# Kernel tuning notes

Hardware: AMD Instinct MI355X
Metric: run time of the kernel (lower is better)

## Reference

```python
import jax, jax.numpy as jnp
import numpy as np

B, C, S, Q = 4, 3, 5, 5
E = 90 * 768          # encoding_size for encoding_method != 1
N1 = B * C * S        # 60 support rows
N2 = B * C * Q        # 60 query rows
H = 32                # width of every Dense layer


def setup_inputs() -> dict:
    key = jax.random.key(0)
    ks = jax.random.split(key, 20)
    p = lambda k, shape: jax.random.normal(k, shape, jnp.float32) * 0.1
    return {
        "support_distance": jax.random.normal(ks[0], (N1, E), jnp.float32),
        "support_label": jax.random.randint(ks[1], (B, 15), 0, C, jnp.int32),
        "query_distance": jax.random.normal(ks[2], (N2, E), jnp.float32),
        # fvc_bar / gvc_bar (shared between distance and label paths)
        "W_fvc_bar": p(ks[3], (1, H)),  "b_fvc_bar": p(ks[4], (H,)),
        "W_gvc_bar": p(ks[5], (H, H)), "b_gvc_bar": p(ks[6], (H,)),
        # fu / gu (input to fu is concat([repeat(32-dim), 1-dim]) -> 33)
        "W_fu": p(ks[7], (H + 1, H)),  "b_fu": p(ks[8], (H,)),
        "W_gu": p(ks[9], (H, H)),      "b_gu": p(ks[10], (H,)),
        # fvc / gvc
        "W_fvc": p(ks[11], (H + 1, H)), "b_fvc": p(ks[12], (H,)),
        "W_gvc": p(ks[13], (H, H)),     "b_gvc": p(ks[14], (H,)),
        # fz / gz
        "W_fz": p(ks[15], (H + 1, H)),  "b_fz": p(ks[16], (H,)),
        "W_gz": p(ks[17], (H, H)),      "b_gz": p(ks[18], (H,)),
    }


def reference(support_distance, support_label, query_distance,
              W_fvc_bar, b_fvc_bar, W_gvc_bar, b_gvc_bar,
              W_fu, b_fu, W_gu, b_gu,
              W_fvc, b_fvc, W_gvc, b_gvc,
              W_fz, b_fz, W_gz, b_gz):
    relu = jax.nn.relu
    d1 = support_distance[..., None]                                   # [N1,E,1]
    # v_bar: fvc_bar over each scalar of the distance, mean over rows, then gvc_bar
    v_bar = relu(jnp.mean(relu(d1 @ W_fvc_bar + b_fvc_bar), axis=0)
                 @ W_gvc_bar + b_gvc_bar)                               # [E,32]
    # c_bar: same stack applied to one-hot labels
    lab = jax.nn.one_hot(support_label.reshape(N1).astype(jnp.int32), C)[..., None]  # [N1,C,1]
    c_bar = relu(jnp.mean(relu(lab @ W_fvc_bar + b_fvc_bar), axis=0)
                 @ W_gvc_bar + b_gvc_bar)                               # [C,32]
    # fu on concat([repeat(v_bar), d1]): split the 33-row weight to avoid concat
    Wu_v, wu_d = W_fu[:H], W_fu[H:]                                     # [32,32],[1,32]
    alpha = jnp.mean(relu((v_bar @ Wu_v)[None] + d1 * wu_d[0] + b_fu), axis=1)  # [N1,32]
    beta = jnp.mean(relu((c_bar @ Wu_v)[None] + lab * wu_d[0] + b_fu), axis=1)  # [N1,32]
    u_n = relu((alpha + beta) @ W_gu + b_gu)                            # [N1,32]
    # fvc on concat([repeat(u_n over E), d1]), mean over rows, gvc
    Wv_u, wv_d = W_fvc[:H], W_fvc[H:]
    v = relu(jnp.mean(relu((u_n @ Wv_u)[:, None, :] + d1 * wv_d[0] + b_fvc),
                      axis=0) @ W_gvc + b_gvc)                          # [E,32]
    # query branch: fz on concat([repeat(v), d2]), mean over E, gz
    d2 = query_distance[..., None]                                      # [N2,E,1]
    Wz_v, wz_d = W_fz[:H], W_fz[H:]
    z = jnp.mean(relu((v @ Wz_v)[None] + d2 * wz_d[0] + b_fz), axis=1)  # [N2,32]
    new_distance = relu(z @ W_gz + b_gz)                                # [N2,32]
    return new_distance.reshape(B, C, Q, H)
```

## Files before the change

### kernel.cpp

```cpp
#include <hip/hip_runtime.h>

#define E_DIM 69120
#define N1 60
#define H 32
#define CC 3
#define TEB 64
#define NB2 (E_DIM / TEB)
#define SDS 65
#define SBT 66
#define PSZ (N1 * H)

#define OFF_R2 (N1 * SDS * 4)
#define OFF_R3 (OFF_R2 + 64 * 33 * 4)
#define SMEM_SZ (OFF_R3 + 64 * 33 * 4)

template<bool ATOMIC>
__global__ __launch_bounds__(256, 4) void kA3(
    const float* __restrict__ d,
    const float* __restrict__ Wfvb, const float* __restrict__ bfvb,
    const float* __restrict__ Wgvb, const float* __restrict__ bgvb,
    const float* __restrict__ Wfu,  const float* __restrict__ bfu,
    float* __restrict__ outp)
{
    __shared__ __align__(16) char smem[SMEM_SZ];
    float* dsf        = (float*)smem;
    float (*bufA)[33] = (float(*)[33])(smem + OFF_R2);
    float (*bufB)[33] = (float(*)[33])(smem + OFF_R3);
    float* bufT       = (float*)(smem + OFF_R2);
    const int tid = threadIdx.x;
    const long sE = (long)blockIdx.x * TEB;

    for (int i = tid; i < N1 * (TEB / 4); i += 256) {
        const int n = i >> 4, c = (i & 15) * 4;
        const float4 v = *(const float4*)(d + (long)n * E_DIM + sE + c);
        float* w = dsf + n * SDS + c;
        w[0] = v.x; w[1] = v.y; w[2] = v.z; w[3] = v.w;
    }
    __syncthreads();

    const int eLoc = tid & 63, h0 = (tid >> 6) * 8;

    {
        float wf[8], bf[8], t1[8];
        #pragma unroll
        for (int j = 0; j < 8; ++j) { wf[j] = Wfvb[h0+j]; bf[j] = bfvb[h0+j]; t1[j] = 0.f; }
        const float* dp = dsf + eLoc;
        #pragma unroll 4
        for (int n = 0; n < N1; ++n) {
            const float dv = dp[n * SDS];
            #pragma unroll
            for (int j = 0; j < 8; ++j) t1[j] += fmaxf(fmaf(dv, wf[j], bf[j]), 0.f);
        }
        #pragma unroll
        for (int j = 0; j < 8; ++j) bufA[eLoc][h0+j] = t1[j] * (1.f / N1);
    }
    __syncthreads();

    {
        float acc[8];
        #pragma unroll
        for (int j = 0; j < 8; ++j) acc[j] = bgvb[h0+j];
        #pragma unroll
        for (int k = 0; k < H; ++k) {
            const float t = bufA[eLoc][k];
            #pragma unroll
            for (int j = 0; j < 8; ++j) acc[j] = fmaf(t, Wgvb[k*H + h0+j], acc[j]);
        }
        #pragma unroll
        for (int j = 0; j < 8; ++j) bufB[eLoc][h0+j] = fmaxf(acc[j], 0.f);
    }
    __syncthreads();

    {
        float acc[8];
        #pragma unroll
        for (int j = 0; j < 8; ++j) acc[j] = bfu[h0+j];
        #pragma unroll
        for (int k = 0; k < H; ++k) {
            const float t = bufB[eLoc][k];
            #pragma unroll
            for (int j = 0; j < 8; ++j) acc[j] = fmaf(t, Wfu[k*H + h0+j], acc[j]);
        }
        #pragma unroll
        for (int j = 0; j < 8; ++j) bufT[(h0+j)*SBT + eLoc] = acc[j];
    }
    __syncthreads();

    if (tid < N1 * 4) {
        const int n = tid >> 2, hb = (tid & 3) * 8;
        float wud[8], acc[8];
        #pragma unroll
        for (int j = 0; j < 8; ++j) { wud[j] = Wfu[H*H + hb + j]; acc[j] = 0.f; }
        const float* drow = d + (long)n * E_DIM + sE;
        for (int e4 = 0; e4 < TEB; e4 += 4) {
            const float4 d4 = *(const float4*)(drow + e4);
            #pragma unroll
            for (int j = 0; j < 8; ++j) {
                const float* wr = bufT + (hb + j) * SBT + e4;
                const float2 wa = *(const float2*)(wr);
                const float2 wb = *(const float2*)(wr + 2);
                acc[j] += fmaxf(fmaf(d4.x, wud[j], wa.x), 0.f)
                        + fmaxf(fmaf(d4.y, wud[j], wa.y), 0.f)
                        + fmaxf(fmaf(d4.z, wud[j], wb.x), 0.f)
                        + fmaxf(fmaf(d4.w, wud[j], wb.y), 0.f);
            }
        }
        if (ATOMIC) {
            float* p = outp + tid * 8;
            #pragma unroll
            for (int j = 0; j < 8; ++j) atomicAdd(&p[j], acc[j]);
        } else {
            float4* p = (float4*)(outp + (long)blockIdx.x * PSZ + tid * 8);
            p[0] = make_float4(acc[0], acc[1], acc[2], acc[3]);
            p[1] = make_float4(acc[4], acc[5], acc[6], acc[7]);
        }
    }
}

template<bool ATOMIC>
__global__ __launch_bounds__(256, 4) void kCf(
    const float* __restrict__ d, const float* __restrict__ d2,
    const float* __restrict__ uwb,
    const float* __restrict__ Wfvc,
    const float* __restrict__ Wgvc, const float* __restrict__ bgvc,
    const float* __restrict__ Wfz,  const float* __restrict__ bfz,
    float* __restrict__ outp)
{
    __shared__ __align__(16) char smem[SMEM_SZ];
    float* dsf        = (float*)smem;
    float (*bufA)[33] = (float(*)[33])(smem + OFF_R2);
    float (*bufB)[33] = (float(*)[33])(smem + OFF_R3);
    float* u_l        = (float*)(smem + OFF_R3);
    float* bufT       = (float*)(smem + OFF_R2);
    const int tid = threadIdx.x;
    const long sE = (long)blockIdx.x * TEB;

    for (int i = tid; i < N1 * (TEB / 4); i += 256) {
        const int n = i >> 4, c = (i & 15) * 4;
        const float4 v = *(const float4*)(d + (long)n * E_DIM + sE + c);
        float* w = dsf + n * SDS + c;
        w[0] = v.x; w[1] = v.y; w[2] = v.z; w[3] = v.w;
    }
    for (int i = tid; i < PSZ / 4; i += 256)
        ((float4*)u_l)[i] = ((const float4*)uwb)[i];
    __syncthreads();

    const int eLoc = tid & 63, h0 = (tid >> 6) * 8;

    {
        float wvd[8], m[8];
        #pragma unroll
        for (int j = 0; j < 8; ++j) { wvd[j] = Wfvc[H*H + h0+j]; m[j] = 0.f; }
        const float* dp = dsf + eLoc;
        #pragma unroll 4
        for (int n = 0; n < N1; ++n) {
            const float dv = dp[n * SDS];
            const float4 u0 = *(const float4*)(u_l + n * H + h0);
            const float4 u1 = *(const float4*)(u_l + n * H + h0 + 4);
            const float ub[8] = {u0.x, u0.y, u0.z, u0.w, u1.x, u1.y, u1.z, u1.w};
            #pragma unroll
            for (int j = 0; j < 8; ++j) m[j] += fmaxf(fmaf(dv, wvd[j], ub[j]), 0.f);
        }
        #pragma unroll
        for (int j = 0; j < 8; ++j) bufA[eLoc][h0+j] = m[j] * (1.f / N1);
    }
    __syncthreads();

    {
        float acc[8];
        #pragma unroll
        for (int j = 0; j < 8; ++j) acc[j] = bgvc[h0+j];
        #pragma unroll
        for (int k = 0; k < H; ++k) {
            const float t = bufA[eLoc][k];
            #pragma unroll
            for (int j = 0; j < 8; ++j) acc[j] = fmaf(t, Wgvc[k*H + h0+j], acc[j]);
        }
        #pragma unroll
        for (int j = 0; j < 8; ++j) bufB[eLoc][h0+j] = fmaxf(acc[j], 0.f);
    }
    __syncthreads();

    {
        float acc[8];
        #pragma unroll
        for (int j = 0; j < 8; ++j) acc[j] = bfz[h0+j];
        #pragma unroll
        for (int k = 0; k < H; ++k) {
            const float t = bufB[eLoc][k];
            #pragma unroll
            for (int j = 0; j < 8; ++j) acc[j] = fmaf(t, Wfz[k*H + h0+j], acc[j]);
        }
        #pragma unroll
        for (int j = 0; j < 8; ++j) bufT[(h0+j)*SBT + eLoc] = acc[j];
    }
    __syncthreads();

    if (tid < N1 * 4) {
        const int n = tid >> 2, hb = (tid & 3) * 8;
        float wzd[8], acc[8];
        #pragma unroll
        for (int j = 0; j < 8; ++j) { wzd[j] = Wfz[H*H + hb + j]; acc[j] = 0.f; }
        const float* drow = d2 + (long)n * E_DIM + sE;
        for (int e4 = 0; e4 < TEB; e4 += 4) {
            const float4 d4 = *(const float4*)(drow + e4);
            #pragma unroll
            for (int j = 0; j < 8; ++j) {
                const float* wr = bufT + (hb + j) * SBT + e4;
                const float2 wa = *(const float2*)(wr);
                const float2 wb = *(const float2*)(wr + 2);
                acc[j] += fmaxf(fmaf(d4.x, wzd[j], wa.x), 0.f)
                        + fmaxf(fmaf(d4.y, wzd[j], wa.y), 0.f)
                        + fmaxf(fmaf(d4.z, wzd[j], wb.x), 0.f)
                        + fmaxf(fmaf(d4.w, wzd[j], wb.y), 0.f);
            }
        }
        if (ATOMIC) {
            float* p = outp + tid * 8;
            #pragma unroll
            for (int j = 0; j < 8; ++j) atomicAdd(&p[j], acc[j]);
        } else {
            float4* p = (float4*)(outp + (long)blockIdx.x * PSZ + tid * 8);
            p[0] = make_float4(acc[0], acc[1], acc[2], acc[3]);
            p[1] = make_float4(acc[4], acc[5], acc[6], acc[7]);
        }
    }
}

__global__ __launch_bounds__(256) void kR(
    const float* __restrict__ part, float* __restrict__ out)
{
    __shared__ float red[16][17];
    const int tid = threadIdx.x;
    const int oLoc = tid & 15, c = tid >> 4;
    const int o = blockIdx.x * 16 + oLoc;
    const int b0 = c * 68;
    const int bN = (NB2 - b0 < 68) ? (NB2 - b0) : 68;
    const float* p = part + (long)b0 * PSZ + o;
    float s = 0.f;
    #pragma unroll 4
    for (int b = 0; b < bN; ++b) s += p[(long)b * PSZ];
    red[c][oLoc] = s;
    __syncthreads();
    if (tid < 16) {
        float t = 0.f;
        #pragma unroll
        for (int ci = 0; ci < 16; ++ci) t += red[ci][tid];
        out[blockIdx.x * 16 + tid] = t;
    }
}

__global__ __launch_bounds__(1024) void kB(
    const float* __restrict__ alphaAcc, const int* __restrict__ label,
    const float* __restrict__ Wfvb, const float* __restrict__ bfvb,
    const float* __restrict__ Wgvb, const float* __restrict__ bgvb,
    const float* __restrict__ Wfu,  const float* __restrict__ bfu,
    const float* __restrict__ Wgu,  const float* __restrict__ bgu,
    const float* __restrict__ Wfvc, const float* __restrict__ bfvc,
    float* __restrict__ uwb)
{
    __shared__ float up_l[N1 * H];
    __shared__ float un_l[N1 * H];
    __shared__ float cb_l[CC * H];
    __shared__ float cw_l[CC * H];
    __shared__ int   cnt[CC];
    const int tid = threadIdx.x;

    if (tid < CC) cnt[tid] = 0;
    __syncthreads();
    if (tid < N1) atomicAdd(&cnt[label[tid]], 1);
    __syncthreads();

    if (tid < CC * H) {
        const int c = tid / H, h = tid % H;
        const float nc = (float)cnt[c];
        float s = bgvb[h];
        #pragma unroll
        for (int k = 0; k < H; ++k) {
            const float t1c = (nc * fmaxf(Wfvb[k] + bfvb[k], 0.f) +
                               ((float)N1 - nc) * fmaxf(bfvb[k], 0.f)) * (1.f / N1);
            s = fmaf(t1c, Wgvb[k * H + h], s);
        }
        cb_l[tid] = fmaxf(s, 0.f);
    }
    __syncthreads();
    if (tid < CC * H) {
        const int c = tid / H, h = tid % H;
        float s = bfu[h];
        #pragma unroll
        for (int k = 0; k < H; ++k) s = fmaf(cb_l[c * H + k], Wfu[k * H + h], s);
        cw_l[tid] = s;
    }
    __syncthreads();
    for (int t = tid; t < N1 * H; t += 1024) {
        const int n = t >> 5, h = t & 31;
        const int ln = label[n];
        const float wud = Wfu[H * H + h];
        float s = 0.f;
        #pragma unroll
        for (int c = 0; c < CC; ++c)
            s += fmaxf(cw_l[c * H + h] + ((c == ln) ? wud : 0.f), 0.f);
        up_l[t] = alphaAcc[t] * (1.f / E_DIM) + s * (1.f / CC);
    }
    __syncthreads();
    for (int t = tid; t < N1 * H; t += 1024) {
        const int n = t >> 5, h = t & 31;
        float s = bgu[h];
        #pragma unroll
        for (int k = 0; k < H; ++k) s = fmaf(up_l[n * H + k], Wgu[k * H + h], s);
        un_l[t] = fmaxf(s, 0.f);
    }
    __syncthreads();
    for (int t = tid; t < N1 * H; t += 1024) {
        const int n = t >> 5, h = t & 31;
        float s = bfvc[h];
        #pragma unroll
        for (int k = 0; k < H; ++k) s = fmaf(un_l[n * H + k], Wfvc[k * H + h], s);
        uwb[t] = s;
    }
}

__global__ __launch_bounds__(1024) void kD(
    const float* __restrict__ zAcc,
    const float* __restrict__ Wgz, const float* __restrict__ bgz,
    float* __restrict__ out)
{
    __shared__ float z_l[N1 * H];
    const int tid = threadIdx.x;
    for (int t = tid; t < N1 * H; t += 1024) z_l[t] = zAcc[t] * (1.f / E_DIM);
    __syncthreads();
    for (int t = tid; t < N1 * H; t += 1024) {
        const int n = t >> 5, h = t & 31;
        float s = bgz[h];
        #pragma unroll
        for (int k = 0; k < H; ++k) s = fmaf(z_l[n * H + k], Wgz[k * H + h], s);
        out[t] = fmaxf(s, 0.f);
    }
}

extern "C" void kernel_launch(void* const* d_in, const int* in_sizes, int n_in,
                              void* d_out, int out_size, void* d_ws, size_t ws_size,
                              hipStream_t stream)
{
    const float* sup  = (const float*)d_in[0];
    const int*   lab  = (const int*)d_in[1];
    const float* qry  = (const float*)d_in[2];
    const float* Wfvb = (const float*)d_in[3];
    const float* bfvb = (const float*)d_in[4];
    const float* Wgvb = (const float*)d_in[5];
    const float* bgvb = (const float*)d_in[6];
    const float* Wfu  = (const float*)d_in[7];
    const float* bfu  = (const float*)d_in[8];
    const float* Wgu  = (const float*)d_in[9];
    const float* bgu  = (const float*)d_in[10];
    const float* Wfvc = (const float*)d_in[11];
    const float* bfvc = (const float*)d_in[12];
    const float* Wgvc = (const float*)d_in[13];
    const float* bgvc = (const float*)d_in[14];
    const float* Wfz  = (const float*)d_in[15];
    const float* bfz  = (const float*)d_in[16];
    const float* Wgz  = (const float*)d_in[17];
    const float* bgz  = (const float*)d_in[18];
    float* out = (float*)d_out;

    float* alphaAcc = (float*)d_ws;
    float* zAcc     = alphaAcc + PSZ;
    float* uwb      = zAcc + PSZ;
    float* partA    = uwb + PSZ;
    float* partZ    = partA + (size_t)NB2 * PSZ;

    const size_t needMain = (3 * (size_t)PSZ + 2 * (size_t)NB2 * PSZ) * sizeof(float);

    if (ws_size >= needMain) {
        kA3<false><<<NB2, 256, 0, stream>>>(sup, Wfvb, bfvb, Wgvb, bgvb, Wfu, bfu, partA);
        kR<<<PSZ / 16, 256, 0, stream>>>(partA, alphaAcc);
        kB<<<1, 1024, 0, stream>>>(alphaAcc, lab, Wfvb, bfvb, Wgvb, bgvb, Wfu, bfu,
                                   Wgu, bgu, Wfvc, bfvc, uwb);
        kCf<false><<<NB2, 256, 0, stream>>>(sup, qry, uwb, Wfvc, Wgvc, bgvc, Wfz, bfz, partZ);
        kR<<<PSZ / 16, 256, 0, stream>>>(partZ, zAcc);
        kD<<<1, 1024, 0, stream>>>(zAcc, Wgz, bgz, out);
    } else {
        (void)hipMemsetAsync(alphaAcc, 0, 2 * PSZ * sizeof(float), stream);
        kA3<true><<<NB2, 256, 0, stream>>>(sup, Wfvb, bfvb, Wgvb, bgvb, Wfu, bfu, alphaAcc);
        kB<<<1, 1024, 0, stream>>>(alphaAcc, lab, Wfvb, bfvb, Wgvb, bgvb, Wfu, bfu,
                                   Wgu, bgu, Wfvc, bfvc, uwb);
        kCf<true><<<NB2, 256, 0, stream>>>(sup, qry, uwb, Wfvc, Wgvc, bgvc, Wfz, bfz, zAcc);
        kD<<<1, 1024, 0, stream>>>(zAcc, Wgz, bgz, out);
    }
}
```

Before: 106.2 us.

## Double threads per block and drop LDS staging of distance tile

Both per-E-tile kernels now run 512 threads, each handling 4 hidden units instead of 8, so parallelism and latency hiding go up. The 60x64 distance tile is no longer staged in shared memory; each thread reads the distance column straight from global memory (coalesced across eLoc). The smaller LDS footprint allows more blocks per CU. The cost is that the later reduction phase rereads the same distance data from global or cache, and every weight element is loaded by twice as many threads.

```diff
diff --git a/kernel.cpp b/kernel.cpp
--- a/kernel.cpp
+++ b/kernel.cpp
@@ -6,97 +6,84 @@
 #define CC 3
 #define TEB 64
 #define NB2 (E_DIM / TEB)
-#define SDS 65
 #define SBT 66
 #define PSZ (N1 * H)
 
-#define OFF_R2 (N1 * SDS * 4)
-#define OFF_R3 (OFF_R2 + 64 * 33 * 4)
-#define SMEM_SZ (OFF_R3 + 64 * 33 * 4)
+#define LDS_FLOATS 4224
 
 template<bool ATOMIC>
-__global__ __launch_bounds__(256, 4) void kA3(
+__global__ __launch_bounds__(512, 4) void kA5(
     const float* __restrict__ d,
     const float* __restrict__ Wfvb, const float* __restrict__ bfvb,
     const float* __restrict__ Wgvb, const float* __restrict__ bgvb,
     const float* __restrict__ Wfu,  const float* __restrict__ bfu,
     float* __restrict__ outp)
 {
-    __shared__ __align__(16) char smem[SMEM_SZ];
-    float* dsf        = (float*)smem;
-    float (*bufA)[33] = (float(*)[33])(smem + OFF_R2);
-    float (*bufB)[33] = (float(*)[33])(smem + OFF_R3);
-    float* bufT       = (float*)(smem + OFF_R2);
+    __shared__ __align__(16) float smem[LDS_FLOATS];
+    float* bufA = smem;
+    float* bufB = smem + 2112;
+    float* bufT = smem;
     const int tid = threadIdx.x;
     const long sE = (long)blockIdx.x * TEB;
-
-    for (int i = tid; i < N1 * (TEB / 4); i += 256) {
-        const int n = i >> 4, c = (i & 15) * 4;
-        const float4 v = *(const float4*)(d + (long)n * E_DIM + sE + c);
-        float* w = dsf + n * SDS + c;
-        w[0] = v.x; w[1] = v.y; w[2] = v.z; w[3] = v.w;
-    }
-    __syncthreads();
-
-    const int eLoc = tid & 63, h0 = (tid >> 6) * 8;
-
-    {
-        float wf[8], bf[8], t1[8];
-        #pragma unroll
-        for (int j = 0; j < 8; ++j) { wf[j] = Wfvb[h0+j]; bf[j] = bfvb[h0+j]; t1[j] = 0.f; }
-        const float* dp = dsf + eLoc;
+    const int eLoc = tid & 63, h0 = (tid >> 6) * 4;
+
+    {
+        float wf[4], bf[4], t1[4];
+        #pragma unroll
+        for (int j = 0; j < 4; ++j) { wf[j] = Wfvb[h0+j]; bf[j] = bfvb[h0+j]; t1[j] = 0.f; }
+        const float* dp = d + sE + eLoc;
         #pragma unroll 4
         for (int n = 0; n < N1; ++n) {
-            const float dv = dp[n * SDS];
-            #pragma unroll
-            for (int j = 0; j < 8; ++j) t1[j] += fmaxf(fmaf(dv, wf[j], bf[j]), 0.f);
-        }
-        #pragma unroll
-        for (int j = 0; j < 8; ++j) bufA[eLoc][h0+j] = t1[j] * (1.f / N1);
-    }
-    __syncthreads();
-
-    {
-        float acc[8];
-        #pragma unroll
-        for (int j = 0; j < 8; ++j) acc[j] = bgvb[h0+j];
-        #pragma unroll
-        for (int k = 0; k < H; ++k) {
-            const float t = bufA[eLoc][k];
-            #pragma unroll
-            for (int j = 0; j < 8; ++j) acc[j] = fmaf(t, Wgvb[k*H + h0+j], acc[j]);
-        }
-        #pragma unroll
-        for (int j = 0; j < 8; ++j) bufB[eLoc][h0+j] = fmaxf(acc[j], 0.f);
-    }
-    __syncthreads();
-
-    {
-        float acc[8];
-        #pragma unroll
-        for (int j = 0; j < 8; ++j) acc[j] = bfu[h0+j];
-        #pragma unroll
-        for (int k = 0; k < H; ++k) {
-            const float t = bufB[eLoc][k];
-            #pragma unroll
-            for (int j = 0; j < 8; ++j) acc[j] = fmaf(t, Wfu[k*H + h0+j], acc[j]);
-        }
-        #pragma unroll
-        for (int j = 0; j < 8; ++j) bufT[(h0+j)*SBT + eLoc] = acc[j];
-    }
-    __syncthreads();
-
-    if (tid < N1 * 4) {
-        const int n = tid >> 2, hb = (tid & 3) * 8;
-        float wud[8], acc[8];
-        #pragma unroll
-        for (int j = 0; j < 8; ++j) { wud[j] = Wfu[H*H + hb + j]; acc[j] = 0.f; }
+            const float dv = dp[(long)n * E_DIM];
+            #pragma unroll
+            for (int j = 0; j < 4; ++j) t1[j] += fmaxf(fmaf(dv, wf[j], bf[j]), 0.f);
+        }
+        #pragma unroll
+        for (int j = 0; j < 4; ++j) bufA[eLoc * 33 + h0 + j] = t1[j] * (1.f / N1);
+    }
+    __syncthreads();
+
+    {
+        float acc[4];
+        #pragma unroll
+        for (int j = 0; j < 4; ++j) acc[j] = bgvb[h0+j];
+        #pragma unroll
+        for (int k = 0; k < H; ++k) {
+            const float t = bufA[eLoc * 33 + k];
+            #pragma unroll
+            for (int j = 0; j < 4; ++j) acc[j] = fmaf(t, Wgvb[k*H + h0+j], acc[j]);
+        }
+        #pragma unroll
+        for (int j = 0; j < 4; ++j) bufB[eLoc * 33 + h0 + j] = fmaxf(acc[j], 0.f);
+    }
+    __syncthreads();
+
+    {
+        float acc[4];
+        #pragma unroll
+        for (int j = 0; j < 4; ++j) acc[j] = bfu[h0+j];
+        #pragma unroll
+        for (int k = 0; k < H; ++k) {
+            const float t = bufB[eLoc * 33 + k];
+            #pragma unroll
+            for (int j = 0; j < 4; ++j) acc[j] = fmaf(t, Wfu[k*H + h0+j], acc[j]);
+        }
+        #pragma unroll
+        for (int j = 0; j < 4; ++j) bufT[(h0+j) * SBT + eLoc] = acc[j];
+    }
+    __syncthreads();
+
+    if (tid < N1 * 8) {
+        const int n = tid >> 3, hb4 = (tid & 7) * 4;
+        float wud[4], acc[4];
+        #pragma unroll
+        for (int j = 0; j < 4; ++j) { wud[j] = Wfu[H*H + hb4 + j]; acc[j] = 0.f; }
         const float* drow = d + (long)n * E_DIM + sE;
         for (int e4 = 0; e4 < TEB; e4 += 4) {
             const float4 d4 = *(const float4*)(drow + e4);
             #pragma unroll
-            for (int j = 0; j < 8; ++j) {
-                const float* wr = bufT + (hb + j) * SBT + e4;
+            for (int j = 0; j < 4; ++j) {
+                const float* wr = bufT + (hb4 + j) * SBT + e4;
                 const float2 wa = *(const float2*)(wr);
                 const float2 wb = *(const float2*)(wr + 2);
                 acc[j] += fmaxf(fmaf(d4.x, wud[j], wa.x), 0.f)
@@ -106,19 +93,18 @@
             }
         }
         if (ATOMIC) {
-            float* p = outp + tid * 8;
-            #pragma unroll
-            for (int j = 0; j < 8; ++j) atomicAdd(&p[j], acc[j]);
+            float* p = outp + n * H + hb4;
+            #pragma unroll
+            for (int j = 0; j < 4; ++j) atomicAdd(&p[j], acc[j]);
         } else {
-            float4* p = (float4*)(outp + (long)blockIdx.x * PSZ + tid * 8);
-            p[0] = make_float4(acc[0], acc[1], acc[2], acc[3]);
-            p[1] = make_float4(acc[4], acc[5], acc[6], acc[7]);
+            *(float4*)(outp + (long)blockIdx.x * PSZ + n * H + hb4) =
+                make_float4(acc[0], acc[1], acc[2], acc[3]);
         }
     }
 }
 
 template<bool ATOMIC>
-__global__ __launch_bounds__(256, 4) void kCf(
+__global__ __launch_bounds__(512, 4) void kCf5(
     const float* __restrict__ d, const float* __restrict__ d2,
     const float* __restrict__ uwb,
     const float* __restrict__ Wfvc,
@@ -126,87 +112,79 @@
     const float* __restrict__ Wfz,  const float* __restrict__ bfz,
     float* __restrict__ outp)
 {
-    __shared__ __align__(16) char smem[SMEM_SZ];
-    float* dsf        = (float*)smem;
-    float (*bufA)[33] = (float(*)[33])(smem + OFF_R2);
-    float (*bufB)[33] = (float(*)[33])(smem + OFF_R3);
-    float* u_l        = (float*)(smem + OFF_R3);
-    float* bufT       = (float*)(smem + OFF_R2);
+    __shared__ __align__(16) float smem[LDS_FLOATS];
+    float* bufA = smem;
+    float* bufB = smem + 2112;
+    float* u_l  = smem + 2112;
+    float* bufT = smem;
     const int tid = threadIdx.x;
     const long sE = (long)blockIdx.x * TEB;
-
-    for (int i = tid; i < N1 * (TEB / 4); i += 256) {
-        const int n = i >> 4, c = (i & 15) * 4;
-        const float4 v = *(const float4*)(d + (long)n * E_DIM + sE + c);
-        float* w = dsf + n * SDS + c;
-        w[0] = v.x; w[1] = v.y; w[2] = v.z; w[3] = v.w;
-    }
-    for (int i = tid; i < PSZ / 4; i += 256)
-        ((float4*)u_l)[i] = ((const float4*)uwb)[i];
-    __syncthreads();
-
-    const int eLoc = tid & 63, h0 = (tid >> 6) * 8;
-
-    {
-        float wvd[8], m[8];
-        #pragma unroll
-        for (int j = 0; j < 8; ++j) { wvd[j] = Wfvc[H*H + h0+j]; m[j] = 0.f; }
-        const float* dp = dsf + eLoc;
+    const int eLoc = tid & 63, h0 = (tid >> 6) * 4;
+
+    if (tid < PSZ / 4)
+        ((float4*)u_l)[tid] = ((const float4*)uwb)[tid];
+    __syncthreads();
+
+    {
+        float wvd[4], m[4];
+        #pragma unroll
+        for (int j = 0; j < 4; ++j) { wvd[j] = Wfvc[H*H + h0+j]; m[j] = 0.f; }
+        const float* dp = d + sE + eLoc;
         #pragma unroll 4
         for (int n = 0; n < N1; ++n) {
-            const float dv = dp[n * SDS];
-            const float4 u0 = *(const float4*)(u_l + n * H + h0);
-            const float4 u1 = *(const float4*)(u_l + n * H + h0 + 4);
-            const float ub[8] = {u0.x, u0.y, u0.z, u0.w, u1.x, u1.y, u1.z, u1.w};
-            #pragma unroll
-            for (int j = 0; j < 8; ++j) m[j] += fmaxf(fmaf(dv, wvd[j], ub[j]), 0.f);
-        }
-        #pragma unroll
-        for (int j = 0; j < 8; ++j) bufA[eLoc][h0+j] = m[j] * (1.f / N1);
-    }
-    __syncthreads();
-
-    {
-        float acc[8];
-        #pragma unroll
-        for (int j = 0; j < 8; ++j) acc[j] = bgvc[h0+j];
-        #pragma unroll
-        for (int k = 0; k < H; ++k) {
-            const float t = bufA[eLoc][k];
-            #pragma unroll
-            for (int j = 0; j < 8; ++j) acc[j] = fmaf(t, Wgvc[k*H + h0+j], acc[j]);
-        }
-        #pragma unroll
-        for (int j = 0; j < 8; ++j) bufB[eLoc][h0+j] = fmaxf(acc[j], 0.f);
-    }
-    __syncthreads();
-
-    {
-        float acc[8];
-        #pragma unroll
-        for (int j = 0; j < 8; ++j) acc[j] = bfz[h0+j];
-        #pragma unroll
-        for (int k = 0; k < H; ++k) {
-            const float t = bufB[eLoc][k];
-            #pragma unroll
-            for (int j = 0; j < 8; ++j) acc[j] = fmaf(t, Wfz[k*H + h0+j], acc[j]);
-        }
-        #pragma unroll
-        for (int j = 0; j < 8; ++j) bufT[(h0+j)*SBT + eLoc] = acc[j];
-    }
-    __syncthreads();
-
-    if (tid < N1 * 4) {
-        const int n = tid >> 2, hb = (tid & 3) * 8;
-        float wzd[8], acc[8];
-        #pragma unroll
-        for (int j = 0; j < 8; ++j) { wzd[j] = Wfz[H*H + hb + j]; acc[j] = 0.f; }
+            const float dv = dp[(long)n * E_DIM];
+            const float4 u4 = *(const float4*)(u_l + n * H + h0);
+            m[0] += fmaxf(fmaf(dv, wvd[0], u4.x), 0.f);
+            m[1] += fmaxf(fmaf(dv, wvd[1], u4.y), 0.f);
+            m[2] += fmaxf(fmaf(dv, wvd[2], u4.z), 0.f);
+            m[3] += fmaxf(fmaf(dv, wvd[3], u4.w), 0.f);
+        }
+        #pragma unroll
+        for (int j = 0; j < 4; ++j) bufA[eLoc * 33 + h0 + j] = m[j] * (1.f / N1);
+    }
+    __syncthreads();
+
+    {
+        float acc[4];
+        #pragma unroll
+        for (int j = 0; j < 4; ++j) acc[j] = bgvc[h0+j];
+        #pragma unroll
+        for (int k = 0; k < H; ++k) {
+            const float t = bufA[eLoc * 33 + k];
+            #pragma unroll
+            for (int j = 0; j < 4; ++j) acc[j] = fmaf(t, Wgvc[k*H + h0+j], acc[j]);
+        }
+        #pragma unroll
+        for (int j = 0; j < 4; ++j) bufB[eLoc * 33 + h0 + j] = fmaxf(acc[j], 0.f);
+    }
+    __syncthreads();
+
+    {
+        float acc[4];
+        #pragma unroll
+        for (int j = 0; j < 4; ++j) acc[j] = bfz[h0+j];
+        #pragma unroll
+        for (int k = 0; k < H; ++k) {
+            const float t = bufB[eLoc * 33 + k];
+            #pragma unroll
+            for (int j = 0; j < 4; ++j) acc[j] = fmaf(t, Wfz[k*H + h0+j], acc[j]);
+        }
+        #pragma unroll
+        for (int j = 0; j < 4; ++j) bufT[(h0+j) * SBT + eLoc] = acc[j];
+    }
+    __syncthreads();
+
+    if (tid < N1 * 8) {
+        const int n = tid >> 3, hb4 = (tid & 7) * 4;
+        float wzd[4], acc[4];
+        #pragma unroll
+        for (int j = 0; j < 4; ++j) { wzd[j] = Wfz[H*H + hb4 + j]; acc[j] = 0.f; }
         const float* drow = d2 + (long)n * E_DIM + sE;
         for (int e4 = 0; e4 < TEB; e4 += 4) {
             const float4 d4 = *(const float4*)(drow + e4);
             #pragma unroll
-            for (int j = 0; j < 8; ++j) {
-                const float* wr = bufT + (hb + j) * SBT + e4;
+            for (int j = 0; j < 4; ++j) {
+                const float* wr = bufT + (hb4 + j) * SBT + e4;
                 const float2 wa = *(const float2*)(wr);
                 const float2 wb = *(const float2*)(wr + 2);
                 acc[j] += fmaxf(fmaf(d4.x, wzd[j], wa.x), 0.f)
@@ -216,13 +194,12 @@
             }
         }
         if (ATOMIC) {
-            float* p = outp + tid * 8;
-            #pragma unroll
-            for (int j = 0; j < 8; ++j) atomicAdd(&p[j], acc[j]);
+            float* p = outp + n * H + hb4;
+            #pragma unroll
+            for (int j = 0; j < 4; ++j) atomicAdd(&p[j], acc[j]);
         } else {
-            float4* p = (float4*)(outp + (long)blockIdx.x * PSZ + tid * 8);
-            p[0] = make_float4(acc[0], acc[1], acc[2], acc[3]);
-            p[1] = make_float4(acc[4], acc[5], acc[6], acc[7]);
+            *(float4*)(outp + (long)blockIdx.x * PSZ + n * H + hb4) =
+                make_float4(acc[0], acc[1], acc[2], acc[3]);
         }
     }
 }
@@ -372,19 +349,19 @@
     const size_t needMain = (3 * (size_t)PSZ + 2 * (size_t)NB2 * PSZ) * sizeof(float);
 
     if (ws_size >= needMain) {
-        kA3<false><<<NB2, 256, 0, stream>>>(sup, Wfvb, bfvb, Wgvb, bgvb, Wfu, bfu, partA);
+        kA5<false><<<NB2, 512, 0, stream>>>(sup, Wfvb, bfvb, Wgvb, bgvb, Wfu, bfu, partA);
         kR<<<PSZ / 16, 256, 0, stream>>>(partA, alphaAcc);
         kB<<<1, 1024, 0, stream>>>(alphaAcc, lab, Wfvb, bfvb, Wgvb, bgvb, Wfu, bfu,
                                    Wgu, bgu, Wfvc, bfvc, uwb);
-        kCf<false><<<NB2, 256, 0, stream>>>(sup, qry, uwb, Wfvc, Wgvc, bgvc, Wfz, bfz, partZ);
+        kCf5<false><<<NB2, 512, 0, stream>>>(sup, qry, uwb, Wfvc, Wgvc, bgvc, Wfz, bfz, partZ);
         kR<<<PSZ / 16, 256, 0, stream>>>(partZ, zAcc);
         kD<<<1, 1024, 0, stream>>>(zAcc, Wgz, bgz, out);
     } else {
         (void)hipMemsetAsync(alphaAcc, 0, 2 * PSZ * sizeof(float), stream);
-        kA3<true><<<NB2, 256, 0, stream>>>(sup, Wfvb, bfvb, Wgvb, bgvb, Wfu, bfu, alphaAcc);
+        kA5<true><<<NB2, 512, 0, stream>>>(sup, Wfvb, bfvb, Wgvb, bgvb, Wfu, bfu, alphaAcc);
         kB<<<1, 1024, 0, stream>>>(alphaAcc, lab, Wfvb, bfvb, Wgvb, bgvb, Wfu, bfu,
                                    Wgu, bgu, Wfvc, bfvc, uwb);
-        kCf<true><<<NB2, 256, 0, stream>>>(sup, qry, uwb, Wfvc, Wgvc, bgvc, Wfz, bfz, zAcc);
+        kCf5<true><<<NB2, 512, 0, stream>>>(sup, qry, uwb, Wfvc, Wgvc, bgvc, Wfz, bfz, zAcc);
         kD<<<1, 1024, 0, stream>>>(zAcc, Wgz, bgz, out);
     }
 }
```

New measurement: 117.4 us. +10.5%, slower.
